# Optimization experiments

Hardware: AMD Instinct MI355X
Metric: run time of the kernel (lower is better)

Reference implementation:

```python
import jax, jax.numpy as jnp
import numpy as np

B, N, C = 4, 2048, 512
H, D, L = 8, 64, 64  # num_heads, per-head dim, lunchbox_dim
SCALE = max(D, L) ** (-0.5)

def setup_inputs() -> dict:
    key = jax.random.key(0)
    k1, k2, k3, k4 = jax.random.split(key, 4)
    x = jax.random.normal(k1, (B, N, C), dtype=jnp.float32)
    v = jax.random.normal(k2, (N, H, L), dtype=jnp.float32) * (1.0 / np.sqrt(N))
    qkv = jax.random.normal(k3, (C, D * 2 * H), dtype=jnp.float32) * (1.0 / np.sqrt(C))
    proj = jax.random.normal(k4, (H * L, D), dtype=jnp.float32) * (1.0 / np.sqrt(H * L))
    return {"x": x, "v": v, "qkv": qkv, "proj": proj}

def reference(x, v, qkv, proj):
    # x: [B,N,C] -> [B,N,H,2,D]
    h = jnp.einsum('bnc,cd->bnd', x, qkv).reshape(B, N, H, 2, D)
    q = h[:, :, :, 0, :]  # [B,N,H,D]
    k = h[:, :, :, 1, :]  # [B,N,H,D]
    # attention scores [B,H,N,N]; NOTE: original code calls tf.nn.softmax but
    # discards the result, so no softmax is applied (faithful reproduction).
    attn = jnp.einsum('bnhd,bmhd->bhnm', q, k) * SCALE
    # contract with batch-independent lunchbox V: [B,H,N,N] x [N,H,L] -> [B,N,H,L]
    res = jnp.einsum('bhnm,mhl->bnhl', attn, v).reshape(B, N, H * L)
    out = jnp.einsum('bnc,cd->bnd', res, proj)  # [B,N,D]
    return out
```

## Files before the change

### kernel.cpp

```cpp
#include <hip/hip_runtime.h>
#include <hip/hip_bf16.h>


using f32x4 = __attribute__((ext_vector_type(4))) float;
using s16x8 = __attribute__((ext_vector_type(8))) short;

__device__ __forceinline__ unsigned short f2bf(float f) {
  unsigned int i;
  __builtin_memcpy(&i, &f, 4);
  unsigned int lsb = (i >> 16) & 1u;
  i += 0x7fffu + lsb;
  return (unsigned short)(i >> 16);
}
__device__ __forceinline__ float bf2f(unsigned short u) {
  unsigned int i = ((unsigned int)u) << 16;
  float f;
  __builtin_memcpy(&f, &i, 4);
  return f;
}
__device__ __forceinline__ void async_cp16(const void* g, void* l) {
  __builtin_amdgcn_global_load_lds((const __attribute__((address_space(1))) void*)g,
                                   (__attribute__((address_space(3))) void*)l, 16, 0, 0);
}

__global__ void k_prep(const float* __restrict__ x, const float* __restrict__ qkv,
                       unsigned short* __restrict__ xb, unsigned short* __restrict__ qkvT) {
  const int id = blockIdx.x;
  const int tid = threadIdx.x;
  if (id < 2048) {
    size_t i = ((size_t)id * 256 + tid) * 8;
    f32x4 a = *(const f32x4*)(x + i);
    f32x4 b = *(const f32x4*)(x + i + 4);
    ushort4 lo, hi;
    lo.x = f2bf(a[0]); lo.y = f2bf(a[1]); lo.z = f2bf(a[2]); lo.w = f2bf(a[3]);
    hi.x = f2bf(b[0]); hi.y = f2bf(b[1]); hi.z = f2bf(b[2]); hi.w = f2bf(b[3]);
    *(ushort4*)(xb + i) = lo;
    *(ushort4*)(xb + i + 4) = hi;
  } else {
    __shared__ float tile[32][33];
    const int idx = id - 2048;
    const int j0 = (idx & 31) * 32;
    const int c0 = (idx >> 5) * 32;
    const int tx = tid & 31, ty = tid >> 5;
#pragma unroll
    for (int i = 0; i < 32; i += 8)
      tile[ty + i][tx] = qkv[(size_t)(c0 + ty + i) * 1024 + j0 + tx];
    __syncthreads();
    const int h = j0 >> 7, s = (j0 >> 6) & 1, d0 = j0 & 63;
    const int jp0 = s * 512 + h * 64 + d0;
#pragma unroll
    for (int i = 0; i < 32; i += 8)
      qkvT[(size_t)(jp0 + ty + i) * 512 + c0 + tx] = f2bf(tile[tx][ty + i]);
  }
}

__global__ __launch_bounds__(512) void k_gemm1(
    const unsigned short* __restrict__ A,
    const unsigned short* __restrict__ Bt,
    unsigned short* __restrict__ Qws,
    unsigned short* __restrict__ Kws) {
  __shared__ unsigned short As[128 * 64];
  __shared__ unsigned short Bs[128 * 64];
  const int lin = blockIdx.x;
  const int wg = (lin & 7) * 64 + (lin >> 3);
  const int m0 = (wg >> 3) * 128;
  const int n0 = (wg & 7) * 128;
  const int tid = threadIdx.x;
  const int lane = tid & 63;
  const int wave = tid >> 6;
  const int wm = wave >> 1, wn = wave & 1;

  f32x4 acc[2][4] = {};

  const int rlane = lane >> 3;
  const int clane = (lane & 7) * 8;

  for (int kt = 0; kt < 512; kt += 64) {
    __syncthreads();
#pragma unroll
    for (int i = 0; i < 2; ++i) {
      async_cp16(A + (size_t)(m0 + i * 64 + wave * 8 + rlane) * 512 + kt + clane,
                 As + (i * 64 + wave * 8) * 64);
      async_cp16(Bt + (size_t)(n0 + i * 64 + wave * 8 + rlane) * 512 + kt + clane,
                 Bs + (i * 64 + wave * 8) * 64);
    }
    __syncthreads();
#pragma unroll
    for (int kk = 0; kk < 64; kk += 32) {
      s16x8 af[2], bfr[4];
#pragma unroll
      for (int i = 0; i < 2; ++i)
        af[i] = *(const s16x8*)(As + (wm * 32 + i * 16 + (lane & 15)) * 64 + kk + (lane >> 4) * 8);
#pragma unroll
      for (int j = 0; j < 4; ++j)
        bfr[j] = *(const s16x8*)(Bs + (wn * 64 + j * 16 + (lane & 15)) * 64 + kk + (lane >> 4) * 8);
#pragma unroll
      for (int i = 0; i < 2; ++i)
#pragma unroll
        for (int j = 0; j < 4; ++j)
          acc[i][j] = __builtin_amdgcn_mfma_f32_16x16x32_bf16(af[i], bfr[j], acc[i][j], 0, 0, 0);
    }
  }
  const int n_base = n0 + wn * 64;
#pragma unroll
  for (int i = 0; i < 2; ++i) {
    int grow = m0 + wm * 32 + i * 16 + (lane >> 4) * 4;
#pragma unroll
    for (int j = 0; j < 4; ++j) {
      int gcol = n_base + j * 16 + (lane & 15);
      unsigned short* dst;
      float scale;
      if (gcol < 512) { dst = Qws; scale = 0.125f; }
      else            { dst = Kws; gcol -= 512; scale = 1.0f; }
#pragma unroll
      for (int r = 0; r < 4; ++r)
        dst[(size_t)(grow + r) * 512 + gcol] = f2bf(acc[i][j][r] * scale);
    }
  }
}

__global__ void k_kv_partial(const unsigned short* __restrict__ Kws,
                             const float* __restrict__ v,
                             float* __restrict__ KVp) {
  const int wg = blockIdx.x;
  const int chunk = wg & 15;
  const int h = (wg >> 4) & 7;
  const int b = wg >> 7;
  __shared__ unsigned short Ks[128 * 64];
  __shared__ float Vs[128 * 64];
  const int tid = threadIdx.x;
  const int lane = tid & 63;
  const int wave = tid >> 6;
  const int n0 = chunk * 128;
  {
    const int r = wave * 32 + (lane >> 3);
    const int c = (lane & 7) * 8;
#pragma unroll
    for (int i = 0; i < 4; ++i)
      async_cp16(Kws + (size_t)(b * 2048 + n0 + r + i * 8) * 512 + h * 64 + c,
                 Ks + (wave * 32 + i * 8) * 64);
  }
  {
    const int r = wave * 32 + (lane >> 4);
    const int c = (lane & 15) * 4;
#pragma unroll
    for (int i = 0; i < 8; ++i)
      async_cp16(v + (size_t)(n0 + r + i * 4) * 512 + h * 64 + c,
                 Vs + (wave * 32 + i * 4) * 64);
  }
  __syncthreads();
  const int dq0 = (tid & 15) * 4;
  const int l0 = (tid >> 4) * 4;
  float acc[4][4] = {};
#pragma unroll 4
  for (int n = 0; n < 128; ++n) {
    ushort4 ku = *(const ushort4*)(Ks + n * 64 + dq0);
    f32x4 va = *(const f32x4*)(Vs + n * 64 + l0);
    float ka[4] = {bf2f(ku.x), bf2f(ku.y), bf2f(ku.z), bf2f(ku.w)};
#pragma unroll
    for (int a = 0; a < 4; ++a)
#pragma unroll
      for (int c = 0; c < 4; ++c)
        acc[a][c] += ka[a] * va[c];
  }
  float* dst = KVp + (size_t)wg * 4096;
#pragma unroll
  for (int a = 0; a < 4; ++a) {
    f32x4 o;
    o[0] = acc[a][0]; o[1] = acc[a][1]; o[2] = acc[a][2]; o[3] = acc[a][3];
    *(f32x4*)(dst + (dq0 + a) * 64 + l0) = o;
  }
}

__global__ void k_w(const float* __restrict__ KVp,
                    const float* __restrict__ proj,
                    unsigned short* __restrict__ WcatT) {
  const int blk = blockIdx.x;
  const int g = blk & 7;
  const int bh = blk >> 3;
  const int h = bh & 7;
  const int b = bh >> 3;
  __shared__ float kv[8 * 64];
  __shared__ float pj[64 * 64];
  const int tid = threadIdx.x;
  {
    const int e = tid * 2;
    const float* src = KVp + (size_t)bh * 16 * 4096 + g * 512 + e;
    float s0 = 0.f, s1 = 0.f;
#pragma unroll
    for (int c = 0; c < 16; ++c) {
      float2 t = *(const float2*)(src + c * 4096);
      s0 += t.x; s1 += t.y;
    }
    kv[e] = s0; kv[e + 1] = s1;
  }
#pragma unroll
  for (int j = 0; j < 16; ++j) {
    int e = tid + j * 256;
    pj[e] = proj[(size_t)h * 4096 + e];
  }
  __syncthreads();
  const int dout = tid & 63;
  const int dq0 = tid >> 6;
  float w0 = 0.f, w1 = 0.f;
  for (int l = 0; l < 64; ++l) {
    float p = pj[l * 64 + dout];
    w0 += kv[dq0 * 64 + l] * p;
    w1 += kv[(dq0 + 4) * 64 + l] * p;
  }
  const int dqb = h * 64 + g * 8;
  WcatT[(size_t)(b * 64 + dout) * 512 + dqb + dq0] = f2bf(w0);
  WcatT[(size_t)(b * 64 + dout) * 512 + dqb + dq0 + 4] = f2bf(w1);
}

__global__ __launch_bounds__(64) void k_gemm2(
    const unsigned short* __restrict__ Qws,
    const unsigned short* __restrict__ WcatT,
    float* __restrict__ out) {
  const int m0 = blockIdx.x * 16;
  const int lane = threadIdx.x;
  const unsigned short* Bb = WcatT + (size_t)(m0 >> 11) * 64 * 512;
  const int arow = lane & 15;
  const int koff = (lane >> 4) * 8;
  f32x4 acc[4] = {};
#pragma unroll
  for (int kk = 0; kk < 16; ++kk) {
    s16x8 af = *(const s16x8*)(Qws + (size_t)(m0 + arow) * 512 + kk * 32 + koff);
#pragma unroll
    for (int j = 0; j < 4; ++j) {
      s16x8 bf = *(const s16x8*)(Bb + (size_t)(j * 16 + arow) * 512 + kk * 32 + koff);
      acc[j] = __builtin_amdgcn_mfma_f32_16x16x32_bf16(af, bf, acc[j], 0, 0, 0);
    }
  }
  const int grow = m0 + (lane >> 4) * 4;
#pragma unroll
  for (int j = 0; j < 4; ++j) {
    int gcol = j * 16 + arow;
#pragma unroll
    for (int r = 0; r < 4; ++r)
      out[(size_t)(grow + r) * 64 + gcol] = acc[j][r];
  }
}

extern "C" void kernel_launch(void* const* d_in, const int* in_sizes, int n_in,
                              void* d_out, int out_size, void* d_ws, size_t ws_size,
                              hipStream_t stream) {
  const float* x    = (const float*)d_in[0];
  const float* v    = (const float*)d_in[1];
  const float* qkv  = (const float*)d_in[2];
  const float* proj = (const float*)d_in[3];
  float* out = (float*)d_out;

  char* ws = (char*)d_ws;
  unsigned short* xb   = (unsigned short*)ws; ws += (size_t)8192 * 512 * 2;
  unsigned short* qkvT = (unsigned short*)ws; ws += (size_t)1024 * 512 * 2;
  unsigned short* Qws  = (unsigned short*)ws; ws += (size_t)8192 * 512 * 2;
  unsigned short* Kws  = (unsigned short*)ws; ws += (size_t)8192 * 512 * 2;
  float*          KVp  = (float*)ws;          ws += (size_t)512 * 4096 * 4;
  unsigned short* Wc   = (unsigned short*)ws; ws += (size_t)4 * 64 * 512 * 2;

  hipLaunchKernelGGL(k_prep, dim3(2560), dim3(256), 0, stream, x, qkv, xb, qkvT);
  hipLaunchKernelGGL(k_gemm1, dim3(512), dim3(512), 0, stream, xb, qkvT, Qws, Kws);
  hipLaunchKernelGGL(k_kv_partial, dim3(512), dim3(256), 0, stream, Kws, v, KVp);
  hipLaunchKernelGGL(k_w, dim3(256), dim3(256), 0, stream, KVp, proj, Wc);
  hipLaunchKernelGGL(k_gemm2, dim3(512), dim3(64), 0, stream, Qws, Wc, out);
}
```

Before: 112.5 us.

## Fuse x bf16 conversion into gemm1 A-loading and store KV partials as bf16

The separate pass that converts x to bf16 is dropped. gemm1 now loads fp32 x into registers, packs it to bf16 and writes it to padded LDS, prefetching the next k-tile's rows while the MFMAs run. This removes a full write and re-read of the bf16 copy of x, and k_prep now only transposes qkv. KV partial sums are also stored as bf16 to halve that traffic, at some cost in precision before the reduction in k_w.

```diff
diff --git a/kernel.cpp b/kernel.cpp
--- a/kernel.cpp
+++ b/kernel.cpp
@@ -18,48 +18,40 @@
   __builtin_memcpy(&f, &i, 4);
   return f;
 }
+__device__ __forceinline__ ushort4 pk4(f32x4 a) {
+  ushort4 u;
+  u.x = f2bf(a[0]); u.y = f2bf(a[1]); u.z = f2bf(a[2]); u.w = f2bf(a[3]);
+  return u;
+}
 __device__ __forceinline__ void async_cp16(const void* g, void* l) {
   __builtin_amdgcn_global_load_lds((const __attribute__((address_space(1))) void*)g,
                                    (__attribute__((address_space(3))) void*)l, 16, 0, 0);
 }
 
-__global__ void k_prep(const float* __restrict__ x, const float* __restrict__ qkv,
-                       unsigned short* __restrict__ xb, unsigned short* __restrict__ qkvT) {
-  const int id = blockIdx.x;
-  const int tid = threadIdx.x;
-  if (id < 2048) {
-    size_t i = ((size_t)id * 256 + tid) * 8;
-    f32x4 a = *(const f32x4*)(x + i);
-    f32x4 b = *(const f32x4*)(x + i + 4);
-    ushort4 lo, hi;
-    lo.x = f2bf(a[0]); lo.y = f2bf(a[1]); lo.z = f2bf(a[2]); lo.w = f2bf(a[3]);
-    hi.x = f2bf(b[0]); hi.y = f2bf(b[1]); hi.z = f2bf(b[2]); hi.w = f2bf(b[3]);
-    *(ushort4*)(xb + i) = lo;
-    *(ushort4*)(xb + i + 4) = hi;
-  } else {
-    __shared__ float tile[32][33];
-    const int idx = id - 2048;
-    const int j0 = (idx & 31) * 32;
-    const int c0 = (idx >> 5) * 32;
-    const int tx = tid & 31, ty = tid >> 5;
-#pragma unroll
-    for (int i = 0; i < 32; i += 8)
-      tile[ty + i][tx] = qkv[(size_t)(c0 + ty + i) * 1024 + j0 + tx];
-    __syncthreads();
-    const int h = j0 >> 7, s = (j0 >> 6) & 1, d0 = j0 & 63;
-    const int jp0 = s * 512 + h * 64 + d0;
-#pragma unroll
-    for (int i = 0; i < 32; i += 8)
-      qkvT[(size_t)(jp0 + ty + i) * 512 + c0 + tx] = f2bf(tile[tx][ty + i]);
-  }
+__global__ void k_prep(const float* __restrict__ qkv, unsigned short* __restrict__ qkvT) {
+  __shared__ float tile[32][33];
+  const int idx = blockIdx.x;
+  const int tid = threadIdx.x;
+  const int j0 = (idx & 31) * 32;
+  const int c0 = (idx >> 5) * 32;
+  const int tx = tid & 31, ty = tid >> 5;
+#pragma unroll
+  for (int i = 0; i < 32; i += 8)
+    tile[ty + i][tx] = qkv[(size_t)(c0 + ty + i) * 1024 + j0 + tx];
+  __syncthreads();
+  const int h = j0 >> 7, s = (j0 >> 6) & 1, d0 = j0 & 63;
+  const int jp0 = s * 512 + h * 64 + d0;
+#pragma unroll
+  for (int i = 0; i < 32; i += 8)
+    qkvT[(size_t)(jp0 + ty + i) * 512 + c0 + tx] = f2bf(tile[tx][ty + i]);
 }
 
 __global__ __launch_bounds__(512) void k_gemm1(
-    const unsigned short* __restrict__ A,
+    const float* __restrict__ X,
     const unsigned short* __restrict__ Bt,
     unsigned short* __restrict__ Qws,
     unsigned short* __restrict__ Kws) {
-  __shared__ unsigned short As[128 * 64];
+  __shared__ unsigned short As[128 * 80];
   __shared__ unsigned short Bs[128 * 64];
   const int lin = blockIdx.x;
   const int wg = (lin & 7) * 64 + (lin >> 3);
@@ -72,25 +64,37 @@
 
   f32x4 acc[2][4] = {};
 
+  const int arow_s = tid >> 4;
+  const int acol_s = (tid & 15) * 4;
   const int rlane = lane >> 3;
   const int clane = (lane & 7) * 8;
 
+  f32x4 areg[4];
+#pragma unroll
+  for (int i = 0; i < 4; ++i)
+    areg[i] = *(const f32x4*)(X + (size_t)(m0 + i * 32 + arow_s) * 512 + acol_s);
+
   for (int kt = 0; kt < 512; kt += 64) {
     __syncthreads();
 #pragma unroll
-    for (int i = 0; i < 2; ++i) {
-      async_cp16(A + (size_t)(m0 + i * 64 + wave * 8 + rlane) * 512 + kt + clane,
-                 As + (i * 64 + wave * 8) * 64);
+    for (int i = 0; i < 2; ++i)
       async_cp16(Bt + (size_t)(n0 + i * 64 + wave * 8 + rlane) * 512 + kt + clane,
                  Bs + (i * 64 + wave * 8) * 64);
-    }
+#pragma unroll
+    for (int i = 0; i < 4; ++i)
+      *(ushort4*)(As + (i * 32 + arow_s) * 80 + acol_s) = pk4(areg[i]);
     __syncthreads();
+    if (kt + 64 < 512) {
+#pragma unroll
+      for (int i = 0; i < 4; ++i)
+        areg[i] = *(const f32x4*)(X + (size_t)(m0 + i * 32 + arow_s) * 512 + kt + 64 + acol_s);
+    }
 #pragma unroll
     for (int kk = 0; kk < 64; kk += 32) {
       s16x8 af[2], bfr[4];
 #pragma unroll
       for (int i = 0; i < 2; ++i)
-        af[i] = *(const s16x8*)(As + (wm * 32 + i * 16 + (lane & 15)) * 64 + kk + (lane >> 4) * 8);
+        af[i] = *(const s16x8*)(As + (wm * 32 + i * 16 + (lane & 15)) * 80 + kk + (lane >> 4) * 8);
 #pragma unroll
       for (int j = 0; j < 4; ++j)
         bfr[j] = *(const s16x8*)(Bs + (wn * 64 + j * 16 + (lane & 15)) * 64 + kk + (lane >> 4) * 8);
@@ -121,7 +125,7 @@
 
 __global__ void k_kv_partial(const unsigned short* __restrict__ Kws,
                              const float* __restrict__ v,
-                             float* __restrict__ KVp) {
+                             unsigned short* __restrict__ KVp) {
   const int wg = blockIdx.x;
   const int chunk = wg & 15;
   const int h = (wg >> 4) & 7;
@@ -163,16 +167,16 @@
       for (int c = 0; c < 4; ++c)
         acc[a][c] += ka[a] * va[c];
   }
-  float* dst = KVp + (size_t)wg * 4096;
+  unsigned short* dst = KVp + (size_t)wg * 4096;
 #pragma unroll
   for (int a = 0; a < 4; ++a) {
     f32x4 o;
     o[0] = acc[a][0]; o[1] = acc[a][1]; o[2] = acc[a][2]; o[3] = acc[a][3];
-    *(f32x4*)(dst + (dq0 + a) * 64 + l0) = o;
-  }
-}
-
-__global__ void k_w(const float* __restrict__ KVp,
+    *(ushort4*)(dst + (dq0 + a) * 64 + l0) = pk4(o);
+  }
+}
+
+__global__ void k_w(const unsigned short* __restrict__ KVp,
                     const float* __restrict__ proj,
                     unsigned short* __restrict__ WcatT) {
   const int blk = blockIdx.x;
@@ -185,12 +189,12 @@
   const int tid = threadIdx.x;
   {
     const int e = tid * 2;
-    const float* src = KVp + (size_t)bh * 16 * 4096 + g * 512 + e;
+    const unsigned short* src = KVp + (size_t)bh * 16 * 4096 + g * 512 + e;
     float s0 = 0.f, s1 = 0.f;
 #pragma unroll
     for (int c = 0; c < 16; ++c) {
-      float2 t = *(const float2*)(src + c * 4096);
-      s0 += t.x; s1 += t.y;
+      ushort2 t = *(const ushort2*)(src + c * 4096);
+      s0 += bf2f(t.x); s1 += bf2f(t.y);
     }
     kv[e] = s0; kv[e + 1] = s1;
   }
@@ -252,15 +256,14 @@
   float* out = (float*)d_out;
 
   char* ws = (char*)d_ws;
-  unsigned short* xb   = (unsigned short*)ws; ws += (size_t)8192 * 512 * 2;
   unsigned short* qkvT = (unsigned short*)ws; ws += (size_t)1024 * 512 * 2;
   unsigned short* Qws  = (unsigned short*)ws; ws += (size_t)8192 * 512 * 2;
   unsigned short* Kws  = (unsigned short*)ws; ws += (size_t)8192 * 512 * 2;
-  float*          KVp  = (float*)ws;          ws += (size_t)512 * 4096 * 4;
+  unsigned short* KVp  = (unsigned short*)ws; ws += (size_t)512 * 4096 * 2;
   unsigned short* Wc   = (unsigned short*)ws; ws += (size_t)4 * 64 * 512 * 2;
 
-  hipLaunchKernelGGL(k_prep, dim3(2560), dim3(256), 0, stream, x, qkv, xb, qkvT);
-  hipLaunchKernelGGL(k_gemm1, dim3(512), dim3(512), 0, stream, xb, qkvT, Qws, Kws);
+  hipLaunchKernelGGL(k_prep, dim3(512), dim3(256), 0, stream, qkv, qkvT);
+  hipLaunchKernelGGL(k_gemm1, dim3(512), dim3(512), 0, stream, x, qkvT, Qws, Kws);
   hipLaunchKernelGGL(k_kv_partial, dim3(512), dim3(256), 0, stream, Kws, v, KVp);
   hipLaunchKernelGGL(k_w, dim3(256), dim3(256), 0, stream, KVp, proj, Wc);
   hipLaunchKernelGGL(k_gemm2, dim3(512), dim3(64), 0, stream, Qws, Wc, out);
```

Result: no change. 112.1 us (-0.4%).
